# Kernel tuning notes

Measured on AMD Instinct MI355X. Metric: run time of the kernel, lower is better.

## Reference

```python
import jax, jax.numpy as jnp
import numpy as np

B, N, C_IN, C_OUT, H_MLP, STEPS, DEG = 8, 128, 512, 512, 128, 10, 16
E = B * N * DEG  # edges per side


def _seg_mean(v, idx, n):
    s = jax.ops.segment_sum(v, idx, num_segments=n)
    c = jax.ops.segment_sum(jnp.ones((v.shape[0], 1), v.dtype), idx, num_segments=n)
    return s / jnp.maximum(c, 1.0)


def _relconv(x, ei, W1, W2, Wr, br):
    n = x.shape[0]
    src, dst = ei[0], ei[1]
    out1 = _seg_mean((x @ W1)[src], dst, n)  # flow source_to_target, mean aggr
    out2 = _seg_mean((x @ W2)[dst], src, n)  # flow target_to_source, mean aggr
    return x @ Wr + br + out1 + out2


def _gnn(x, ei, p):
    # GNNForEmbedding: 1 RelConv layer, LayerNorm(relu(.)), cat=True, lin=True (eval: dropout off)
    W1, W2, Wr, br, g, b, Fw, Fb = p
    h = jax.nn.relu(_relconv(x, ei, W1, W2, Wr, br))
    mu = h.mean(-1, keepdims=True)
    var = ((h - mu) ** 2).mean(-1, keepdims=True)
    h = (h - mu) / jnp.sqrt(var + 1e-5) * g + b
    return jnp.concatenate([x, h], -1) @ Fw + Fb


def setup_inputs():
    key = jax.random.key(0)
    ks = jax.random.split(key, 20)
    nn_ = B * N

    def randn(k, shape, s=1.0):
        return jax.random.normal(k, shape, jnp.float32) * s

    def mk_edges(k):
        k1, k2 = jax.random.split(k)
        off = jnp.repeat(jnp.arange(B, dtype=jnp.int32) * N, N * DEG)
        src = jax.random.randint(k1, (E,), 0, N, jnp.int32) + off
        dst = jax.random.randint(k2, (E,), 0, N, jnp.int32) + off
        return jnp.stack([src, dst])

    s = 0.04
    inp = {
        'x_s': randn(ks[0], (nn_, C_IN)),
        'edge_index_s': mk_edges(ks[1]),
        'edge_attr_s': randn(ks[2], (E, 1)),
        'batch_s': jnp.repeat(jnp.arange(B, dtype=jnp.int32), N),
        'x_t': randn(ks[3], (nn_, C_IN)),
        'edge_index_t': mk_edges(ks[4]),
        'edge_attr_t': randn(ks[5], (E, 1)),
        'batch_t': jnp.repeat(jnp.arange(B, dtype=jnp.int32), N),
        'e_lin1': randn(ks[6], (C_IN, C_OUT), s),
        'e_lin2': randn(ks[7], (C_IN, C_OUT), s),
        'e_rw': randn(ks[8], (C_IN, C_OUT), s),
        'e_rb': jnp.zeros((C_OUT,), jnp.float32),
        'e_g': jnp.ones((C_OUT,), jnp.float32),
        'e_b': jnp.zeros((C_OUT,), jnp.float32),
        'e_fw': randn(ks[9], (C_IN + C_OUT, C_OUT), s),
        'e_fb': jnp.zeros((C_OUT,), jnp.float32),
        'c_lin1': randn(ks[10], (C_IN, C_OUT), s),
        'c_lin2': randn(ks[11], (C_IN, C_OUT), s),
        'c_rw': randn(ks[12], (C_IN, C_OUT), s),
        'c_rb': jnp.zeros((C_OUT,), jnp.float32),
        'c_g': jnp.ones((C_OUT,), jnp.float32),
        'c_b': jnp.zeros((C_OUT,), jnp.float32),
        'c_fw': randn(ks[13], (C_IN + C_OUT, C_OUT), s),
        'c_fb': jnp.zeros((C_OUT,), jnp.float32),
        'm_w1': randn(ks[14], (C_OUT, H_MLP), s),
        'm_b1': jnp.zeros((H_MLP,), jnp.float32),
        'm_w2': randn(ks[15], (H_MLP,), s),
        'm_b2': jnp.zeros((), jnp.float32),
    }
    return inp


def reference(x_s, edge_index_s, edge_attr_s, batch_s, x_t, edge_index_t, edge_attr_t, batch_t,
              e_lin1, e_lin2, e_rw, e_rb, e_g, e_b, e_fw, e_fb,
              c_lin1, c_lin2, c_rw, c_rb, c_g, c_b, c_fw, c_fb,
              m_w1, m_b1, m_w2, m_b2):
    pe = (e_lin1, e_lin2, e_rw, e_rb, e_g, e_b, e_fw, e_fb)
    pc = (c_lin1, c_lin2, c_rw, c_rb, c_g, c_b, c_fw, c_fb)
    # embedding GNN (detached in original model)
    Hs = jax.lax.stop_gradient(_gnn(x_s, edge_index_s, pe)).reshape(B, N, C_OUT)
    Ht = jax.lax.stop_gradient(_gnn(x_t, edge_index_t, pe)).reshape(B, N, C_OUT)
    # all graphs have exactly N nodes -> masks are all-True, masked_softmax == softmax
    S_hat = jnp.einsum('bsc,btc->bst', Hs, Ht)
    S_0 = jax.nn.softmax(S_hat, axis=-1).reshape(B * N, N)
    rkey = jax.random.key(42)
    for t in range(STEPS):
        S = jax.nn.softmax(S_hat, axis=-1)
        R_s = jax.random.normal(jax.random.fold_in(rkey, t), (B, N, C_IN), jnp.float32)
        R_t = jnp.einsum('bst,bsc->btc', S, R_s)  # S^T @ R_s
        O_s = _gnn(R_s.reshape(-1, C_IN), edge_index_s, pc).reshape(B, N, C_OUT)
        O_t = _gnn(R_t.reshape(-1, C_IN), edge_index_t, pc).reshape(B, N, C_OUT)
        # fc1(O_s_i - O_t_j) = O_s_i@W1 - O_t_j@W1 + b1 (linearity): avoid O(Ns*Nt*C) diff tensor
        A = O_s @ m_w1 + m_b1          # [B, Ns, H]
        Bm = O_t @ m_w1                # [B, Nt, H]
        hid = jax.nn.relu(A[:, :, None, :] - Bm[:, None, :, :])  # [B, Ns, Nt, H]
        S_hat = S_hat + (hid @ m_w2 + m_b2)
    S_L = jax.nn.softmax(S_hat, axis=-1).reshape(B * N, N)
    return (S_0, S_L)
```

## Files before the change

kernel.cpp:

```cpp
#include <hip/hip_runtime.h>
#include <stdint.h>


typedef unsigned short u16;
typedef unsigned int u32;
typedef __attribute__((ext_vector_type(8))) short short8;
typedef __attribute__((ext_vector_type(4))) float f32x4;

__device__ inline u16 f2bf(float x) {
  u32 u = __float_as_uint(x);
  u32 r = (u + 0x7fffu + ((u >> 16) & 1u)) >> 16;
  return (u16)r;
}
__device__ inline float bf2f(u16 h) { return __uint_as_float(((u32)h) << 16); }
__device__ inline void split2(float x, u16& h, u16& l) {
  h = f2bf(x);
  l = f2bf(x - bf2f(h));
}

__host__ __device__ inline void tf2x32(uint32_t k0, uint32_t k1, uint32_t x0,
                                       uint32_t x1, uint32_t& o0, uint32_t& o1) {
  uint32_t ks0 = k0, ks1 = k1, ks2 = 0x1BD11BDAu ^ k0 ^ k1;
  x0 += ks0; x1 += ks1;
#define TF_R(r) { x0 += x1; x1 = (x1 << r) | (x1 >> (32 - r)); x1 ^= x0; }
  TF_R(13) TF_R(15) TF_R(26) TF_R(6)   x0 += ks1; x1 += ks2 + 1u;
  TF_R(17) TF_R(29) TF_R(16) TF_R(24)  x0 += ks2; x1 += ks0 + 2u;
  TF_R(13) TF_R(15) TF_R(26) TF_R(6)   x0 += ks0; x1 += ks1 + 3u;
  TF_R(17) TF_R(29) TF_R(16) TF_R(24)  x0 += ks1; x1 += ks2 + 4u;
  TF_R(13) TF_R(15) TF_R(26) TF_R(6)   x0 += ks2; x1 += ks0 + 5u;
#undef TF_R
  o0 = x0; o1 = x1;
}

__device__ inline float erfinv_f(float x) {
  float w = -log1pf(-x * x);
  float p;
  if (w < 5.0f) {
    w = w - 2.5f;
    p = 2.81022636e-08f;
    p = fmaf(p, w, 3.43273939e-07f);
    p = fmaf(p, w, -3.5233877e-06f);
    p = fmaf(p, w, -4.39150654e-06f);
    p = fmaf(p, w, 0.00021858087f);
    p = fmaf(p, w, -0.00125372503f);
    p = fmaf(p, w, -0.00417768164f);
    p = fmaf(p, w, 0.246640727f);
    p = fmaf(p, w, 1.50140941f);
  } else {
    w = sqrtf(w) - 3.0f;
    p = -0.000200214257f;
    p = fmaf(p, w, 0.000100950558f);
    p = fmaf(p, w, 0.00134934322f);
    p = fmaf(p, w, -0.00367342844f);
    p = fmaf(p, w, 0.00573950773f);
    p = fmaf(p, w, -0.0076224613f);
    p = fmaf(p, w, 0.00943887047f);
    p = fmaf(p, w, 1.00167406f);
    p = fmaf(p, w, 2.83297682f);
  }
  return p * x;
}

__device__ inline float bits_to_normal(uint32_t bits) {
  uint32_t fb = (bits >> 9) | 0x3f800000u;
  float f = __uint_as_float(fb) - 1.0f;
  float u = f * 2.0f + (-0.99999994f);
  u = fmaxf(-0.99999994f, u);
  return 1.41421356f * erfinv_f(u);
}

template <int OUTP, int BIASN, int BIASM, int AGGB, int PADD>
__global__ __launch_bounds__(256) void mfma_gemm(
    int K,
    const u16* __restrict__ Ah, const u16* __restrict__ Al, int lda, int sA,
    const u16* __restrict__ Bh, const u16* __restrict__ Bl, int ldb, int sB,
    float* __restrict__ Cf, u16* __restrict__ Ch, u16* __restrict__ Cl,
    int ldc, int sC, const float* __restrict__ bias,
    const u16* __restrict__ Padh, const u16* __restrict__ Padl) {
  const int g = blockIdx.z;
  Ah += (size_t)g * sA; Al += (size_t)g * sA;
  Bh += (size_t)g * sB; Bl += (size_t)g * sB;
  if (OUTP) { Ch += (size_t)g * sC; Cl += (size_t)g * sC; }
  else { Cf += (size_t)g * sC; }
  __shared__ u16 As[2][64][64];
  __shared__ u16 Bs[2][64][64];
  const int tid = threadIdx.x;
  const int m0 = blockIdx.y * 64, n0 = blockIdx.x * 64;
  const int l = tid & 63;
  const int w = tid >> 6;
  const int wr = (w >> 1) * 32, wc = (w & 1) * 32;
  const int l15 = l & 15, lq = l >> 4;
  f32x4 acc[2][2] = {};
  const int sr = tid >> 3, sc = tid & 7;
  for (int k0 = 0; k0 < K; k0 += 64) {
    __syncthreads();
#pragma unroll
    for (int p = 0; p < 2; ++p) {
      int r = sr + p * 32;
      int dst = (sc ^ (r & 7)) * 8;
      *(uint4*)&As[0][r][dst] = *(const uint4*)&Ah[(size_t)(m0 + r) * lda + k0 + sc * 8];
      *(uint4*)&As[1][r][dst] = *(const uint4*)&Al[(size_t)(m0 + r) * lda + k0 + sc * 8];
      size_t boff;
      if (AGGB) {
        int rowg = (k0 < 128) ? (n0 + r) : (512 + n0 + r);
        boff = (size_t)rowg * ldb + (k0 & 127) + sc * 8;
      } else {
        boff = (size_t)(n0 + r) * ldb + k0 + sc * 8;
      }
      *(uint4*)&Bs[0][r][dst] = *(const uint4*)&Bh[boff];
      *(uint4*)&Bs[1][r][dst] = *(const uint4*)&Bl[boff];
    }
    __syncthreads();
#pragma unroll
    for (int kk = 0; kk < 2; ++kk) {
      short8 aH[2], aL[2], bH[2], bL[2];
#pragma unroll
      for (int i = 0; i < 2; ++i) {
        int mr = wr + i * 16 + l15;
        int ca = ((kk * 4 + lq) ^ (mr & 7)) * 8;
        aH[i] = *(const short8*)&As[0][mr][ca];
        aL[i] = *(const short8*)&As[1][mr][ca];
        int nr = wc + i * 16 + l15;
        int cb = ((kk * 4 + lq) ^ (nr & 7)) * 8;
        bH[i] = *(const short8*)&Bs[0][nr][cb];
        bL[i] = *(const short8*)&Bs[1][nr][cb];
      }
#pragma unroll
      for (int i = 0; i < 2; ++i)
#pragma unroll
        for (int j = 0; j < 2; ++j) {
          acc[i][j] = __builtin_amdgcn_mfma_f32_16x16x32_bf16(aH[i], bH[j], acc[i][j], 0, 0, 0);
          acc[i][j] = __builtin_amdgcn_mfma_f32_16x16x32_bf16(aL[i], bH[j], acc[i][j], 0, 0, 0);
          acc[i][j] = __builtin_amdgcn_mfma_f32_16x16x32_bf16(aH[i], bL[j], acc[i][j], 0, 0, 0);
        }
    }
  }
#pragma unroll
  for (int i = 0; i < 2; ++i)
#pragma unroll
    for (int j = 0; j < 2; ++j) {
      int n = n0 + wc + j * 16 + l15;
      int mb = m0 + wr + i * 16 + lq * 4;
      f32x4 v = acc[i][j];
      if (BIASN) {
        float b = bias[n];
        v[0] += b; v[1] += b; v[2] += b; v[3] += b;
      }
      if (BIASM) {
        f32x4 bb = *(const f32x4*)&bias[mb];
        v[0] += bb[0]; v[1] += bb[1]; v[2] += bb[2]; v[3] += bb[3];
      }
      if (PADD) {
        uint2 ph = *(const uint2*)&Padh[(size_t)n * 2048 + mb];
        uint2 pl = *(const uint2*)&Padl[(size_t)n * 2048 + mb];
        v[0] += bf2f((u16)(ph.x & 0xffff)) + bf2f((u16)(pl.x & 0xffff));
        v[1] += bf2f((u16)(ph.x >> 16)) + bf2f((u16)(pl.x >> 16));
        v[2] += bf2f((u16)(ph.y & 0xffff)) + bf2f((u16)(pl.y & 0xffff));
        v[3] += bf2f((u16)(ph.y >> 16)) + bf2f((u16)(pl.y >> 16));
      }
      if (OUTP) {
        u16 h[4], lo[4];
        split2(v[0], h[0], lo[0]); split2(v[1], h[1], lo[1]);
        split2(v[2], h[2], lo[2]); split2(v[3], h[3], lo[3]);
        uint2 hv = {(u32)h[0] | ((u32)h[1] << 16), (u32)h[2] | ((u32)h[3] << 16)};
        uint2 lv = {(u32)lo[0] | ((u32)lo[1] << 16), (u32)lo[2] | ((u32)lo[3] << 16)};
        *(uint2*)&Ch[(size_t)n * ldc + mb] = hv;
        *(uint2*)&Cl[(size_t)n * ldc + mb] = lv;
      } else {
        *(f32x4*)&Cf[(size_t)n * ldc + mb] = v;
      }
    }
}

__global__ __launch_bounds__(256) void count_kernel(const int* __restrict__ ei_s,
                                                    const int* __restrict__ ei_t,
                                                    int* __restrict__ Acnt,
                                                    int* __restrict__ degd,
                                                    int* __restrict__ degs) {
  int e = blockIdx.x * 256 + threadIdx.x;
  int side = e >> 14, idx = e & 16383;
  const int* ei = side ? ei_t : ei_s;
  int src = ei[idx], dst = ei[16384 + idx];
  int g = (dst >> 7) + side * 8;
  int dl = dst & 127, sl = src & 127;
  atomicAdd(&Acnt[(g * 128 + dl) * 128 + sl], 1);
  atomicAdd(&degd[g * 128 + dl], 1);
  atomicAdd(&degs[g * 128 + sl], 1);
}

__global__ __launch_bounds__(256) void norm_adj_kernel(const int* __restrict__ Acnt,
                                                       const int* __restrict__ degd,
                                                       const int* __restrict__ degs,
                                                       u16* __restrict__ Mh,
                                                       u16* __restrict__ Ml) {
  int idx = blockIdx.x * 256 + threadIdx.x;
  int g = idx >> 15, m = (idx >> 8) & 127, k = idx & 255;
  float val;
  if (k < 128)
    val = (float)Acnt[(g * 128 + m) * 128 + k] / (float)max(degd[g * 128 + m], 1);
  else
    val = (float)Acnt[(g * 128 + (k - 128)) * 128 + m] / (float)max(degs[g * 128 + m], 1);
  u16 h, lo;
  split2(val, h, lo);
  Mh[idx] = h; Ml[idx] = lo;
}

__global__ __launch_bounds__(256) void convert_packed(const float* __restrict__ W1,
                                                      const float* __restrict__ W2,
                                                      const float* __restrict__ Wr,
                                                      u16* __restrict__ Th,
                                                      u16* __restrict__ Tl) {
  int id = blockIdx.x * 256 + threadIdx.x;
  int n = id >> 9, k = id & 511;
  const float* W = (n < 512) ? W1 : ((n < 1024) ? W2 : Wr);
  float v = W[k * 512 + (n & 511)];
  u16 h, lo;
  split2(v, h, lo);
  Th[id] = h; Tl[id] = lo;
}

__global__ __launch_bounds__(256) void convert_wT(const float* __restrict__ W,
                                                  u16* __restrict__ Th,
                                                  u16* __restrict__ Tl,
                                                  int K, int N) {
  int id = blockIdx.x * 256 + threadIdx.x;
  int k = id / N, n = id - k * N;
  u16 h, lo;
  split2(W[id], h, lo);
  Th[n * K + k] = h;
  Tl[n * K + k] = lo;
}

__global__ __launch_bounds__(256) void fm_split(const float* __restrict__ Fm,
                                                u16* __restrict__ WFTch,
                                                u16* __restrict__ WFTcl,
                                                u16* __restrict__ FmTrh,
                                                u16* __restrict__ FmTrl) {
  int id = blockIdx.x * 256 + threadIdx.x;
  int k = id >> 7, h = id & 127;
  float v = Fm[k * 128 + h];
  u16 hi, lo;
  split2(v, hi, lo);
  if (k < 512) {
    WFTch[(size_t)(1536 + h) * 512 + k] = hi;
    WFTcl[(size_t)(1536 + h) * 512 + k] = lo;
  } else {
    FmTrh[(size_t)h * 512 + (k - 512)] = hi;
    FmTrl[(size_t)h * 512 + (k - 512)] = lo;
  }
}

__global__ __launch_bounds__(128) void fbm_kernel(const float* __restrict__ fb,
                                                  const float* __restrict__ w1,
                                                  const float* __restrict__ b1,
                                                  float* __restrict__ fbm) {
  int h = threadIdx.x;
  float acc = b1[h];
  for (int c = 0; c < 512; ++c) acc = fmaf(fb[c], w1[c * 128 + h], acc);
  fbm[h] = acc;
}

__global__ __launch_bounds__(256) void copyx_kernel(const float* __restrict__ xs,
                                                    const float* __restrict__ xt,
                                                    u16* __restrict__ XHh,
                                                    u16* __restrict__ XHl) {
  int idx = blockIdx.x * 256 + threadIdx.x;
  int row = idx >> 7, c4 = (idx & 127) << 2;
  const float* src = (row < 1024) ? (xs + row * 512 + c4)
                                  : (xt + (row - 1024) * 512 + c4);
  float4 v = *(const float4*)src;
  u16 h[4], lo[4];
  split2(v.x, h[0], lo[0]); split2(v.y, h[1], lo[1]);
  split2(v.z, h[2], lo[2]); split2(v.w, h[3], lo[3]);
  uint2 hv = {(u32)h[0] | ((u32)h[1] << 16), (u32)h[2] | ((u32)h[3] << 16)};
  uint2 lv = {(u32)lo[0] | ((u32)lo[1] << 16), (u32)lo[2] | ((u32)lo[3] << 16)};
  *(uint2*)&XHh[row * 1024 + c4] = hv;
  *(uint2*)&XHl[row * 1024 + c4] = lv;
}

__global__ __launch_bounds__(256) void gemm_f32(
    int M, int N, int K,
    const float* __restrict__ A, int lda,
    const float* __restrict__ B, int ldb,
    float* __restrict__ C, int ldc) {
  int m0 = blockIdx.y * 64, n0 = blockIdx.x * 64;
  __shared__ float As[16][64];
  __shared__ float Bs[16][64];
  int tid = threadIdx.x;
  int tx = tid & 15, ty = tid >> 4;
  float acc[4][4] = {};
  for (int k0 = 0; k0 < K; k0 += 16) {
    {
      int m_l = tid & 63, k_l = (tid >> 6) << 2;
      float4 av = *(const float4*)&A[(m0 + m_l) * lda + k0 + k_l];
      As[k_l + 0][m_l] = av.x; As[k_l + 1][m_l] = av.y;
      As[k_l + 2][m_l] = av.z; As[k_l + 3][m_l] = av.w;
    }
    {
      int k_l = tid >> 4, n_l = (tid & 15) << 2;
      float4 bv = *(const float4*)&B[(k0 + k_l) * ldb + n0 + n_l];
      *(float4*)&Bs[k_l][n_l] = bv;
    }
    __syncthreads();
#pragma unroll
    for (int kk = 0; kk < 16; ++kk) {
      float4 a4 = *(const float4*)&As[kk][ty << 2];
      float4 b4 = *(const float4*)&Bs[kk][tx << 2];
      float av[4] = {a4.x, a4.y, a4.z, a4.w};
      float bv[4] = {b4.x, b4.y, b4.z, b4.w};
#pragma unroll
      for (int i = 0; i < 4; ++i)
#pragma unroll
        for (int j = 0; j < 4; ++j) acc[i][j] = fmaf(av[i], bv[j], acc[i][j]);
    }
    __syncthreads();
  }
#pragma unroll
  for (int i = 0; i < 4; ++i) {
    int m = m0 + (ty << 2) + i;
    float4 v = {acc[i][0], acc[i][1], acc[i][2], acc[i][3]};
    *(float4*)&C[m * ldc + n0 + (tx << 2)] = v;
  }
}

__global__ __launch_bounds__(256) void ln_stats(
    const u16* __restrict__ Yth, const u16* __restrict__ Ytl,
    const float* __restrict__ AGGt, const float* __restrict__ rb,
    float* __restrict__ partS, float* __restrict__ partQ) {
  int cg = blockIdx.x, ng = blockIdx.y;
  int lane = threadIdx.x & 63, cs = threadIdx.x >> 6;
  int node = ng * 64 + lane;
  float s = 0.f, q = 0.f;
#pragma unroll
  for (int k = 0; k < 16; ++k) {
    int c = cg * 64 + cs * 16 + k;
    size_t yi = (size_t)(1024 + c) * 2048 + node;
    float v = bf2f(Yth[yi]) + bf2f(Ytl[yi]) + rb[c] + AGGt[(size_t)c * 2048 + node];
    v = fmaxf(v, 0.f);
    s += v; q += v * v;
  }
  __shared__ float ls[4][64], lq[4][64];
  ls[cs][lane] = s; lq[cs][lane] = q;
  __syncthreads();
  if (cs == 0) {
    s = ls[0][lane] + ls[1][lane] + ls[2][lane] + ls[3][lane];
    q = lq[0][lane] + lq[1][lane] + lq[2][lane] + lq[3][lane];
    partS[cg * 2048 + node] = s;
    partQ[cg * 2048 + node] = q;
  }
}

__global__ __launch_bounds__(256) void ln_apply(
    const u16* __restrict__ Yth, const u16* __restrict__ Ytl,
    const float* __restrict__ AGGt, const float* __restrict__ partS,
    const float* __restrict__ partQ, const float* __restrict__ rb,
    const float* __restrict__ gam, const float* __restrict__ bet,
    u16* __restrict__ XHh, u16* __restrict__ XHl) {
  int cg = blockIdx.x, ng = blockIdx.y;
  int lane = threadIdx.x & 63, cs = threadIdx.x >> 6;
  int node = ng * 64 + lane;
  float s = 0.f, q = 0.f;
#pragma unroll
  for (int p = 0; p < 8; ++p) {
    s += partS[p * 2048 + node];
    q += partQ[p * 2048 + node];
  }
  float mu = s * (1.f / 512.f);
  float var = q * (1.f / 512.f) - mu * mu;
  float inv = 1.f / sqrtf(var + 1e-5f);
  __shared__ u16 oth[64][66], otl[64][66];
#pragma unroll
  for (int k = 0; k < 16; ++k) {
    int c = cg * 64 + cs * 16 + k;
    size_t yi = (size_t)(1024 + c) * 2048 + node;
    float v = bf2f(Yth[yi]) + bf2f(Ytl[yi]) + rb[c] + AGGt[(size_t)c * 2048 + node];
    v = fmaxf(v, 0.f);
    float o = (v - mu) * inv * gam[c] + bet[c];
    u16 h, lo;
    split2(o, h, lo);
    oth[lane][cs * 16 + k] = h;
    otl[lane][cs * 16 + k] = lo;
  }
  __syncthreads();
  int nl = threadIdx.x >> 2, cq = (threadIdx.x & 3) * 16;
  size_t xbase = (size_t)(ng * 64 + nl) * 1024 + 512 + cg * 64 + cq;
  uint4 h0, h1, l0, l1;
  h0 = *(const uint4*)&oth[nl][cq];     h1 = *(const uint4*)&oth[nl][cq + 8];
  l0 = *(const uint4*)&otl[nl][cq];     l1 = *(const uint4*)&otl[nl][cq + 8];
  *(uint4*)&XHh[xbase] = h0;  *(uint4*)&XHh[xbase + 8] = h1;
  *(uint4*)&XHl[xbase] = l0;  *(uint4*)&XHl[xbase + 8] = l1;
}

__global__ __launch_bounds__(256) void srk_kernel(
    const float* __restrict__ SH, u16* __restrict__ STh, u16* __restrict__ STl,
    u16* __restrict__ XHh, u16* __restrict__ XHl,
    float* __restrict__ outp, u32 k0, u32 k1) {
  int bid = blockIdx.x;
  int tid = threadIdx.x;
  if (bid < 512) {
    int r = bid * 2 + (tid >> 7);
    int t = tid & 127;
    int gg = r >> 7, s = r & 127;
    float a = SH[r * 128 + t];
    float m = a;
#pragma unroll
    for (int off = 32; off > 0; off >>= 1) m = fmaxf(m, __shfl_xor(m, off));
    __shared__ float red[2][4];
    int wv = tid >> 6;
    if ((tid & 63) == 0) red[0][wv] = m;
    __syncthreads();
    m = fmaxf(red[0][wv], red[0][wv ^ 1]);
    float e = expf(a - m);
    float su = e;
#pragma unroll
    for (int off = 32; off > 0; off >>= 1) su += __shfl_xor(su, off);
    if ((tid & 63) == 0) red[1][wv] = su;
    __syncthreads();
    su = red[1][wv] + red[1][wv ^ 1];
    float p = e / su;
    u16 h, lo;
    split2(p, h, lo);
    STh[(gg * 128 + t) * 128 + s] = h;
    STl[(gg * 128 + t) * 128 + s] = lo;
    if (outp) outp[r * 128 + t] = p;
  } else {
    u32 j = (u32)(bid - 512) * 256 + tid;
    u32 o0, o1;
    tf2x32(k0, k1, 0u, j, o0, o1);
    float val = bits_to_normal(o0 ^ o1);
    u32 node = j >> 9, ch = j & 511;
    u16 h, lo;
    split2(val, h, lo);
    XHh[node * 1024 + ch] = h;
    XHl[node * 1024 + ch] = lo;
  }
}

__global__ __launch_bounds__(128) void dist_kernel(const float* __restrict__ Pt,
                                                   const float* __restrict__ b1,
                                                   const float* __restrict__ w2,
                                                   const float* __restrict__ b2,
                                                   float* __restrict__ SH) {
  int bs = blockIdx.x;
  int gb = bs >> 7;
  int t = threadIdx.x;
  __shared__ float arow[128], w2s[128];
  arow[t] = Pt[(size_t)t * 2048 + bs] + b1[t];
  w2s[t] = w2[t];
  __syncthreads();
  const float* pt = Pt + 1024 + gb * 128 + t;
  float acc = 0.f;
#pragma unroll 8
  for (int h = 0; h < 128; ++h) {
    float pv = pt[(size_t)h * 2048];
    acc += fmaxf(arow[h] - pv, 0.f) * w2s[h];
  }
  SH[bs * 128 + t] += acc + b2[0];
}

extern "C" void kernel_launch(void* const* d_in, const int* in_sizes, int n_in,
                              void* d_out, int out_size, void* d_ws, size_t ws_size,
                              hipStream_t stream) {
  const float* x_s = (const float*)d_in[0];
  const int* ei_s = (const int*)d_in[1];
  const float* x_t = (const float*)d_in[4];
  const int* ei_t = (const int*)d_in[5];
  const float* e_lin1 = (const float*)d_in[8];
  const float* e_lin2 = (const float*)d_in[9];
  const float* e_rw = (const float*)d_in[10];
  const float* e_rb = (const float*)d_in[11];
  const float* e_g = (const float*)d_in[12];
  const float* e_b = (const float*)d_in[13];
  const float* e_fw = (const float*)d_in[14];
  const float* e_fb = (const float*)d_in[15];
  const float* c_lin1 = (const float*)d_in[16];
  const float* c_lin2 = (const float*)d_in[17];
  const float* c_rw = (const float*)d_in[18];
  const float* c_rb = (const float*)d_in[19];
  const float* c_g = (const float*)d_in[20];
  const float* c_b = (const float*)d_in[21];
  const float* c_fw = (const float*)d_in[22];
  const float* c_fb = (const float*)d_in[23];
  const float* m_w1 = (const float*)d_in[24];
  const float* m_b1 = (const float*)d_in[25];
  const float* m_w2 = (const float*)d_in[26];
  const float* m_b2 = (const float*)d_in[27];
  float* out = (float*)d_out;
  float* ws = (float*)d_ws;

  u16* Mch   = (u16*)(ws + 0);
  u16* Mcl   = (u16*)(ws + 262144);
  u16* Yth   = (u16*)(ws + 524288);
  u16* Ytl   = (u16*)(ws + 2228224);
  float* AGGt = ws + 3932160;
  u16* XHh   = (u16*)(ws + 4980736);
  u16* XHl   = (u16*)(ws + 6029312);
  u16* WTeh  = (u16*)(ws + 7077888);
  u16* WTel  = (u16*)(ws + 7471104);
  u16* WFTch = (u16*)(ws + 7864320);
  u16* WFTcl = (u16*)(ws + 8290304);
  u16* FTeh  = (u16*)(ws + 8716288);
  u16* FTel  = (u16*)(ws + 8978432);
  u16* FmTrh = (u16*)(ws + 9240576);
  u16* FmTrl = (u16*)(ws + 9273344);
  u16* Oh    = (u16*)(ws + 9306112);
  u16* Ol    = (u16*)(ws + 9830400);
  u16* STh   = (u16*)(ws + 10354688);
  u16* STl   = (u16*)(ws + 10420224);
  float* SH  = ws + 10485760;
  float* Pt  = ws + 10616832;
  float* Fm  = ws + 10878976;
  float* fbm = ws + 11010048;
  float* partS = ws + 11010176;
  float* partQ = ws + 11026560;
  int* Acnt  = (int*)Yth;
  int* degd  = Acnt + 262144;
  int* degs  = degd + 2048;

  hipMemsetAsync(Acnt, 0, (262144 + 4096) * sizeof(int), stream);
  count_kernel<<<128, 256, 0, stream>>>(ei_s, ei_t, Acnt, degd, degs);
  norm_adj_kernel<<<2048, 256, 0, stream>>>(Acnt, degd, degs, Mch, Mcl);
  convert_packed<<<3072, 256, 0, stream>>>(e_lin1, e_lin2, e_rw, WTeh, WTel);
  convert_packed<<<3072, 256, 0, stream>>>(c_lin1, c_lin2, c_rw, WFTch, WFTcl);
  convert_wT<<<2048, 256, 0, stream>>>(e_fw, FTeh, FTel, 1024, 512);
  gemm_f32<<<dim3(2, 16, 1), 256, 0, stream>>>(1024, 128, 512, c_fw, 512,
                                               m_w1, 128, Fm, 128);
  fm_split<<<512, 256, 0, stream>>>(Fm, WFTch, WFTcl, FmTrh, FmTrl);
  fbm_kernel<<<1, 128, 0, stream>>>(c_fb, m_w1, m_b1, fbm);
  copyx_kernel<<<1024, 256, 0, stream>>>(x_s, x_t, XHh, XHl);

  mfma_gemm<1, 0, 0, 0, 0><<<dim3(24, 32, 1), 256, 0, stream>>>(
      512, XHh, XHl, 1024, 0, WTeh, WTel, 512, 0,
      nullptr, Yth, Ytl, 2048, 0, nullptr, nullptr, nullptr);
  mfma_gemm<0, 0, 0, 1, 0><<<dim3(8, 2, 16), 256, 0, stream>>>(
      256, Mch, Mcl, 256, 32768, Yth, Ytl, 2048, 128,
      AGGt, nullptr, nullptr, 2048, 128, nullptr, nullptr, nullptr);
  ln_stats<<<dim3(8, 32), 256, 0, stream>>>(Yth, Ytl, AGGt, e_rb, partS, partQ);
  ln_apply<<<dim3(8, 32), 256, 0, stream>>>(Yth, Ytl, AGGt, partS, partQ,
                                            e_rb, e_g, e_b, XHh, XHl);
  mfma_gemm<1, 0, 1, 0, 0><<<dim3(32, 8, 1), 256, 0, stream>>>(
      1024, FTeh, FTel, 1024, 0, XHh, XHl, 1024, 0,
      nullptr, Oh, Ol, 512, 0, e_fb, nullptr, nullptr);
  mfma_gemm<0, 0, 0, 0, 0><<<dim3(2, 2, 8), 256, 0, stream>>>(
      512, Oh + 1024 * 512, Ol + 1024 * 512, 512, 128 * 512,
      Oh, Ol, 512, 128 * 512,
      SH, nullptr, nullptr, 128, 16384, nullptr, nullptr, nullptr);

  {
    uint32_t fk0, fk1;
    tf2x32(0u, 42u, 0u, 0u, fk0, fk1);
    srk_kernel<<<2560, 256, 0, stream>>>(SH, STh, STl, XHh, XHl, out, fk0, fk1);
  }

  for (int t = 0; t < 10; ++t) {
    mfma_gemm<1, 0, 0, 0, 0><<<dim3(26, 16, 1), 256, 0, stream>>>(
        512, XHh, XHl, 1024, 0, WFTch, WFTcl, 512, 0,
        nullptr, Yth, Ytl, 2048, 0, nullptr, nullptr, nullptr);
    mfma_gemm<1, 0, 0, 0, 0><<<dim3(26, 2, 8), 256, 0, stream>>>(
        128, STh, STl, 128, 16384, Yth, Ytl, 2048, 128,
        nullptr, Yth + 1024, Ytl + 1024, 2048, 128, nullptr, nullptr, nullptr);
    mfma_gemm<0, 0, 0, 1, 0><<<dim3(8, 2, 16), 256, 0, stream>>>(
        256, Mch, Mcl, 256, 32768, Yth, Ytl, 2048, 128,
        AGGt, nullptr, nullptr, 2048, 128, nullptr, nullptr, nullptr);
    ln_stats<<<dim3(8, 32), 256, 0, stream>>>(Yth, Ytl, AGGt, c_rb, partS, partQ);
    ln_apply<<<dim3(8, 32), 256, 0, stream>>>(Yth, Ytl, AGGt, partS, partQ,
                                              c_rb, c_g, c_b, XHh, XHl);
    mfma_gemm<0, 1, 0, 0, 1><<<dim3(2, 32, 1), 256, 0, stream>>>(
        512, XHh + 512, XHl + 512, 1024, 0, FmTrh, FmTrl, 512, 0,
        Pt, nullptr, nullptr, 2048, 0, fbm,
        Yth + (size_t)1536 * 2048, Ytl + (size_t)1536 * 2048);
    dist_kernel<<<1024, 128, 0, stream>>>(Pt, m_b1, m_w2, m_b2, SH);
    uint32_t fk0, fk1;
    tf2x32(0u, 42u, 0u, (uint32_t)(t + 1), fk0, fk1);
    srk_kernel<<<(t < 9) ? 2560 : 512, 256, 0, stream>>>(
        SH, STh, STl, XHh, XHl, (t == 9) ? (out + 131072) : nullptr, fk0, fk1);
  }
}
```

Measured before the change: 858.0 us.

## Fuse LayerNorm into downstream GEMM epilogue and fold gamma/beta into weights

In the iterative loop, the aggregation GEMM is transposed so it writes node-major relu(h) directly, adding the root-weight term and bias in its epilogue. A small row-stats kernel computes the LayerNorm sums. The normalization is then applied algebraically in the epilogue of the following fc GEMM, using gamma folded into the weights plus precomputed sg and cbf vectors. This removes the separate ln_stats/ln_apply passes and one write of normalized activations. The cost is a one-pass variance (E[x²]-mu²), which may lose precision, and strided scalar reads of Y in the relu epilogue.

Result: faster. 841.0 us (-2.0%).

```diff
diff --git a/kernel.cpp b/kernel.cpp
--- a/kernel.cpp
+++ b/kernel.cpp
@@ -69,14 +69,18 @@
   return 1.41421356f * erfinv_f(u);
 }
 
-template <int OUTP, int BIASN, int BIASM, int AGGB, int PADD>
+template <int OUTP, int BIASN, int BIASM, int AGGB, int PADD, int AGGA,
+          int RELUV, int LNEP>
 __global__ __launch_bounds__(256) void mfma_gemm(
     int K,
     const u16* __restrict__ Ah, const u16* __restrict__ Al, int lda, int sA,
     const u16* __restrict__ Bh, const u16* __restrict__ Bl, int ldb, int sB,
     float* __restrict__ Cf, u16* __restrict__ Ch, u16* __restrict__ Cl,
     int ldc, int sC, const float* __restrict__ bias,
-    const u16* __restrict__ Padh, const u16* __restrict__ Padl) {
+    const u16* __restrict__ Padh, const u16* __restrict__ Padl,
+    const u16* __restrict__ Yrh, const u16* __restrict__ Yrl,
+    const float* __restrict__ rbv, const float* __restrict__ pS,
+    const float* __restrict__ pQ, const float* __restrict__ sgv) {
   const int g = blockIdx.z;
   Ah += (size_t)g * sA; Al += (size_t)g * sA;
   Bh += (size_t)g * sB; Bl += (size_t)g * sB;
@@ -98,8 +102,15 @@
     for (int p = 0; p < 2; ++p) {
       int r = sr + p * 32;
       int dst = (sc ^ (r & 7)) * 8;
-      *(uint4*)&As[0][r][dst] = *(const uint4*)&Ah[(size_t)(m0 + r) * lda + k0 + sc * 8];
-      *(uint4*)&As[1][r][dst] = *(const uint4*)&Al[(size_t)(m0 + r) * lda + k0 + sc * 8];
+      size_t aoff;
+      if (AGGA) {
+        int rowg = (k0 < 128) ? (m0 + r) : (512 + m0 + r);
+        aoff = (size_t)rowg * lda + (k0 & 127) + sc * 8;
+      } else {
+        aoff = (size_t)(m0 + r) * lda + k0 + sc * 8;
+      }
+      *(uint4*)&As[0][r][dst] = *(const uint4*)&Ah[aoff];
+      *(uint4*)&As[1][r][dst] = *(const uint4*)&Al[aoff];
       size_t boff;
       if (AGGB) {
         int rowg = (k0 < 128) ? (n0 + r) : (512 + n0 + r);
@@ -150,6 +161,19 @@
         f32x4 bb = *(const f32x4*)&bias[mb];
         v[0] += bb[0]; v[1] += bb[1]; v[2] += bb[2]; v[3] += bb[3];
       }
+      if (LNEP) {
+        f32x4 ps = *(const f32x4*)&pS[mb];
+        f32x4 pq = *(const f32x4*)&pQ[mb];
+        float sgh = sgv[n];
+        float cbh = bias[n];
+#pragma unroll
+        for (int r = 0; r < 4; ++r) {
+          float mu = ps[r] * (1.f / 512.f);
+          float var = pq[r] * (1.f / 512.f) - mu * mu;
+          float inv = 1.f / sqrtf(var + 1e-5f);
+          v[r] = inv * (v[r] - mu * sgh) + cbh;
+        }
+      }
       if (PADD) {
         uint2 ph = *(const uint2*)&Padh[(size_t)n * 2048 + mb];
         uint2 pl = *(const uint2*)&Padl[(size_t)n * 2048 + mb];
@@ -157,6 +181,15 @@
         v[1] += bf2f((u16)(ph.x >> 16)) + bf2f((u16)(pl.x >> 16));
         v[2] += bf2f((u16)(ph.y & 0xffff)) + bf2f((u16)(pl.y & 0xffff));
         v[3] += bf2f((u16)(ph.y >> 16)) + bf2f((u16)(pl.y >> 16));
+      }
+      if (RELUV) {
+        int ngl = g * 128 + n;
+        f32x4 rbq = *(const f32x4*)&rbv[mb];
+#pragma unroll
+        for (int r = 0; r < 4; ++r) {
+          size_t yi = (size_t)(1024 + mb + r) * 2048 + ngl;
+          v[r] = fmaxf(v[r] + bf2f(Yrh[yi]) + bf2f(Yrl[yi]) + rbq[r], 0.f);
+        }
       }
       if (OUTP) {
         u16 h[4], lo[4];
@@ -232,32 +265,41 @@
 }
 
 __global__ __launch_bounds__(256) void fm_split(const float* __restrict__ Fm,
+                                                const float* __restrict__ cg,
                                                 u16* __restrict__ WFTch,
                                                 u16* __restrict__ WFTcl,
-                                                u16* __restrict__ FmTrh,
-                                                u16* __restrict__ FmTrl) {
+                                                u16* __restrict__ FgTh,
+                                                u16* __restrict__ FgTl) {
   int id = blockIdx.x * 256 + threadIdx.x;
   int k = id >> 7, h = id & 127;
   float v = Fm[k * 128 + h];
   u16 hi, lo;
-  split2(v, hi, lo);
   if (k < 512) {
+    split2(v, hi, lo);
     WFTch[(size_t)(1536 + h) * 512 + k] = hi;
     WFTcl[(size_t)(1536 + h) * 512 + k] = lo;
   } else {
-    FmTrh[(size_t)h * 512 + (k - 512)] = hi;
-    FmTrl[(size_t)h * 512 + (k - 512)] = lo;
-  }
-}
-
-__global__ __launch_bounds__(128) void fbm_kernel(const float* __restrict__ fb,
-                                                  const float* __restrict__ w1,
-                                                  const float* __restrict__ b1,
-                                                  float* __restrict__ fbm) {
+    split2(v * cg[k - 512], hi, lo);
+    FgTh[(size_t)h * 512 + (k - 512)] = hi;
+    FgTl[(size_t)h * 512 + (k - 512)] = lo;
+  }
+}
+
+__global__ __launch_bounds__(128) void sgcbf_kernel(
+    const float* __restrict__ Fm, const float* __restrict__ cg,
+    const float* __restrict__ cb, const float* __restrict__ cfb,
+    const float* __restrict__ w1, const float* __restrict__ b1,
+    float* __restrict__ sg, float* __restrict__ cbf) {
   int h = threadIdx.x;
-  float acc = b1[h];
-  for (int c = 0; c < 512; ++c) acc = fmaf(fb[c], w1[c * 128 + h], acc);
-  fbm[h] = acc;
+  float s = 0.f, c2 = 0.f, fb = b1[h];
+  for (int c = 0; c < 512; ++c) {
+    float fm = Fm[(512 + c) * 128 + h];
+    s = fmaf(cg[c], fm, s);
+    c2 = fmaf(cb[c], fm, c2);
+    fb = fmaf(cfb[c], w1[c * 128 + h], fb);
+  }
+  sg[h] = s;
+  cbf[h] = c2 + fb;
 }
 
 __global__ __launch_bounds__(256) void copyx_kernel(const float* __restrict__ xs,
@@ -389,6 +431,34 @@
   l0 = *(const uint4*)&otl[nl][cq];     l1 = *(const uint4*)&otl[nl][cq + 8];
   *(uint4*)&XHh[xbase] = h0;  *(uint4*)&XHh[xbase + 8] = h1;
   *(uint4*)&XHl[xbase] = l0;  *(uint4*)&XHl[xbase + 8] = l1;
+}
+
+__global__ __launch_bounds__(256) void ln_stats_v(
+    const u16* __restrict__ vh, const u16* __restrict__ vl,
+    float* __restrict__ pSv, float* __restrict__ pQv) {
+  int node = blockIdx.x * 8 + (threadIdx.x >> 5);
+  int l32 = threadIdx.x & 31;
+  size_t base = (size_t)node * 512 + l32 * 16;
+  uint4 h0 = *(const uint4*)&vh[base];
+  uint4 h1 = *(const uint4*)&vh[base + 8];
+  uint4 l0 = *(const uint4*)&vl[base];
+  uint4 l1 = *(const uint4*)&vl[base + 8];
+  float s = 0.f, q = 0.f;
+  u32 hw[8] = {h0.x, h0.y, h0.z, h0.w, h1.x, h1.y, h1.z, h1.w};
+  u32 lw[8] = {l0.x, l0.y, l0.z, l0.w, l1.x, l1.y, l1.z, l1.w};
+#pragma unroll
+  for (int i = 0; i < 8; ++i) {
+    float a = bf2f((u16)(hw[i] & 0xffff)) + bf2f((u16)(lw[i] & 0xffff));
+    float b = bf2f((u16)(hw[i] >> 16)) + bf2f((u16)(lw[i] >> 16));
+    s += a + b;
+    q += a * a + b * b;
+  }
+#pragma unroll
+  for (int off = 16; off > 0; off >>= 1) {
+    s += __shfl_xor(s, off);
+    q += __shfl_xor(q, off);
+  }
+  if (l32 == 0) { pSv[node] = s; pQv[node] = q; }
 }
 
 __global__ __launch_bounds__(256) void srk_kernel(
@@ -501,8 +571,8 @@
   u16* WFTcl = (u16*)(ws + 8290304);
   u16* FTeh  = (u16*)(ws + 8716288);
   u16* FTel  = (u16*)(ws + 8978432);
-  u16* FmTrh = (u16*)(ws + 9240576);
-  u16* FmTrl = (u16*)(ws + 9273344);
+  u16* FgTh  = (u16*)(ws + 9240576);
+  u16* FgTl  = (u16*)(ws + 9273344);
   u16* Oh    = (u16*)(ws + 9306112);
   u16* Ol    = (u16*)(ws + 9830400);
   u16* STh   = (u16*)(ws + 10354688);
@@ -510,9 +580,12 @@
   float* SH  = ws + 10485760;
   float* Pt  = ws + 10616832;
   float* Fm  = ws + 10878976;
-  float* fbm = ws + 11010048;
-  float* partS = ws + 11010176;
-  float* partQ = ws + 11026560;
+  float* sg  = ws + 11010048;
+  float* cbf = ws + 11010176;
+  float* partS = ws + 11010304;
+  float* partQ = ws + 11026688;
+  float* pSv = ws + 11043072;
+  float* pQv = ws + 11045120;
   int* Acnt  = (int*)Yth;
   int* degd  = Acnt + 262144;
   int* degs  = degd + 2048;
@@ -525,26 +598,30 @@
   convert_wT<<<2048, 256, 0, stream>>>(e_fw, FTeh, FTel, 1024, 512);
   gemm_f32<<<dim3(2, 16, 1), 256, 0, stream>>>(1024, 128, 512, c_fw, 512,
                                                m_w1, 128, Fm, 128);
-  fm_split<<<512, 256, 0, stream>>>(Fm, WFTch, WFTcl, FmTrh, FmTrl);
-  fbm_kernel<<<1, 128, 0, stream>>>(c_fb, m_w1, m_b1, fbm);
+  fm_split<<<512, 256, 0, stream>>>(Fm, c_g, WFTch, WFTcl, FgTh, FgTl);
+  sgcbf_kernel<<<1, 128, 0, stream>>>(Fm, c_g, c_b, c_fb, m_w1, m_b1, sg, cbf);
   copyx_kernel<<<1024, 256, 0, stream>>>(x_s, x_t, XHh, XHl);
 
-  mfma_gemm<1, 0, 0, 0, 0><<<dim3(24, 32, 1), 256, 0, stream>>>(
+  mfma_gemm<1, 0, 0, 0, 0, 0, 0, 0><<<dim3(24, 32, 1), 256, 0, stream>>>(
       512, XHh, XHl, 1024, 0, WTeh, WTel, 512, 0,
-      nullptr, Yth, Ytl, 2048, 0, nullptr, nullptr, nullptr);
-  mfma_gemm<0, 0, 0, 1, 0><<<dim3(8, 2, 16), 256, 0, stream>>>(
+      nullptr, Yth, Ytl, 2048, 0, nullptr, nullptr, nullptr,
+      nullptr, nullptr, nullptr, nullptr, nullptr, nullptr);
+  mfma_gemm<0, 0, 0, 1, 0, 0, 0, 0><<<dim3(8, 2, 16), 256, 0, stream>>>(
       256, Mch, Mcl, 256, 32768, Yth, Ytl, 2048, 128,
-      AGGt, nullptr, nullptr, 2048, 128, nullptr, nullptr, nullptr);
+      AGGt, nullptr, nullptr, 2048, 128, nullptr, nullptr, nullptr,
+      nullptr, nullptr, nullptr, nullptr, nullptr, nullptr);
   ln_stats<<<dim3(8, 32), 256, 0, stream>>>(Yth, Ytl, AGGt, e_rb, partS, partQ);
   ln_apply<<<dim3(8, 32), 256, 0, stream>>>(Yth, Ytl, AGGt, partS, partQ,
                                             e_rb, e_g, e_b, XHh, XHl);
-  mfma_gemm<1, 0, 1, 0, 0><<<dim3(32, 8, 1), 256, 0, stream>>>(
+  mfma_gemm<1, 0, 1, 0, 0, 0, 0, 0><<<dim3(32, 8, 1), 256, 0, stream>>>(
       1024, FTeh, FTel, 1024, 0, XHh, XHl, 1024, 0,
-      nullptr, Oh, Ol, 512, 0, e_fb, nullptr, nullptr);
-  mfma_gemm<0, 0, 0, 0, 0><<<dim3(2, 2, 8), 256, 0, stream>>>(
+      nullptr, Oh, Ol, 512, 0, e_fb, nullptr, nullptr,
+      nullptr, nullptr, nullptr, nullptr, nullptr, nullptr);
+  mfma_gemm<0, 0, 0, 0, 0, 0, 0, 0><<<dim3(2, 2, 8), 256, 0, stream>>>(
       512, Oh + 1024 * 512, Ol + 1024 * 512, 512, 128 * 512,
       Oh, Ol, 512, 128 * 512,
-      SH, nullptr, nullptr, 128, 16384, nullptr, nullptr, nullptr);
+      SH, nullptr, nullptr, 128, 16384, nullptr, nullptr, nullptr,
+      nullptr, nullptr, nullptr, nullptr, nullptr, nullptr);
 
   {
     uint32_t fk0, fk1;
@@ -553,22 +630,24 @@
   }
 
   for (int t = 0; t < 10; ++t) {
-    mfma_gemm<1, 0, 0, 0, 0><<<dim3(26, 16, 1), 256, 0, stream>>>(
+    mfma_gemm<1, 0, 0, 0, 0, 0, 0, 0><<<dim3(26, 16, 1), 256, 0, stream>>>(
         512, XHh, XHl, 1024, 0, WFTch, WFTcl, 512, 0,
-        nullptr, Yth, Ytl, 2048, 0, nullptr, nullptr, nullptr);
-    mfma_gemm<1, 0, 0, 0, 0><<<dim3(26, 2, 8), 256, 0, stream>>>(
+        nullptr, Yth, Ytl, 2048, 0, nullptr, nullptr, nullptr,
+        nullptr, nullptr, nullptr, nullptr, nullptr, nullptr);
+    mfma_gemm<1, 0, 0, 0, 0, 0, 0, 0><<<dim3(26, 2, 8), 256, 0, stream>>>(
         128, STh, STl, 128, 16384, Yth, Ytl, 2048, 128,
-        nullptr, Yth + 1024, Ytl + 1024, 2048, 128, nullptr, nullptr, nullptr);
-    mfma_gemm<0, 0, 0, 1, 0><<<dim3(8, 2, 16), 256, 0, stream>>>(
-        256, Mch, Mcl, 256, 32768, Yth, Ytl, 2048, 128,
-        AGGt, nullptr, nullptr, 2048, 128, nullptr, nullptr, nullptr);
-    ln_stats<<<dim3(8, 32), 256, 0, stream>>>(Yth, Ytl, AGGt, c_rb, partS, partQ);
-    ln_apply<<<dim3(8, 32), 256, 0, stream>>>(Yth, Ytl, AGGt, partS, partQ,
-                                              c_rb, c_g, c_b, XHh, XHl);
-    mfma_gemm<0, 1, 0, 0, 1><<<dim3(2, 32, 1), 256, 0, stream>>>(
-        512, XHh + 512, XHl + 512, 1024, 0, FmTrh, FmTrl, 512, 0,
-        Pt, nullptr, nullptr, 2048, 0, fbm,
-        Yth + (size_t)1536 * 2048, Ytl + (size_t)1536 * 2048);
+        nullptr, Yth + 1024, Ytl + 1024, 2048, 128, nullptr, nullptr, nullptr,
+        nullptr, nullptr, nullptr, nullptr, nullptr, nullptr);
+    mfma_gemm<1, 0, 0, 0, 0, 1, 1, 0><<<dim3(2, 8, 16), 256, 0, stream>>>(
+        256, Yth, Ytl, 2048, 128, Mch, Mcl, 256, 32768,
+        nullptr, Oh, Ol, 512, 128 * 512, nullptr, nullptr, nullptr,
+        Yth, Ytl, c_rb, nullptr, nullptr, nullptr);
+    ln_stats_v<<<256, 256, 0, stream>>>(Oh, Ol, pSv, pQv);
+    mfma_gemm<0, 0, 0, 0, 1, 0, 0, 1><<<dim3(2, 32, 1), 256, 0, stream>>>(
+        512, Oh, Ol, 512, 0, FgTh, FgTl, 512, 0,
+        Pt, nullptr, nullptr, 2048, 0, cbf,
+        Yth + (size_t)1536 * 2048, Ytl + (size_t)1536 * 2048,
+        nullptr, nullptr, nullptr, pSv, pQv, sg);
     dist_kernel<<<1024, 128, 0, stream>>>(Pt, m_b1, m_w2, m_b2, SH);
     uint32_t fk0, fk1;
     tf2x32(0u, 42u, 0u, (uint32_t)(t + 1), fk0, fk1);
```
